# Kernel optimization log

Hardware: AMD Instinct MI355X
Metric: run time of the kernel (lower is better)

The kernel has to match this reference:

```python
import jax, jax.numpy as jnp
import numpy as np

R_S, R_C, P, L, NVOX, CH = 48, 144, 27, 2, 128, 128


def encode(x, L=L):
    # NeRF-style positional encoding: [sin(2^l x), cos(2^l x)] for l in range(L)
    feats = []
    for l in range(L):
        f = (2.0 ** l) * x
        feats.append(jnp.sin(f))
        feats.append(jnp.cos(f))
    return jnp.concatenate(feats, axis=-1)


def setup_inputs() -> dict:
    key = jax.random.key(0)
    ks = jax.random.split(key, 8)
    Np = 524288
    xyz = jax.random.uniform(ks[0], (Np, 3), dtype=jnp.float32)          # inside bbox [0,1]^3
    directions = jax.random.normal(ks[1], (Np, 3), dtype=jnp.float32)
    # voxel grid buffer: linspace over bbox per axis -> (3, NVOX)
    voxel = jnp.stack([jnp.linspace(0.0, 1.0, NVOX)] * 3, axis=0).astype(jnp.float32)
    sigma = 0.1 * jax.random.normal(ks[2], (3, R_S, NVOX), dtype=jnp.float32)
    feature = 0.1 * jax.random.normal(ks[3], (3, R_C, NVOX), dtype=jnp.float32)
    B = jax.random.normal(ks[4], (R_C, P), dtype=jnp.float32)
    din = (P + 3) * L * 2  # 120
    W1 = jax.random.normal(ks[5], (din, CH), dtype=jnp.float32) / jnp.sqrt(din)
    b1 = jnp.zeros((CH,), jnp.float32)
    W2 = jax.random.normal(ks[6], (CH, CH), dtype=jnp.float32) / jnp.sqrt(CH)
    b2 = jnp.zeros((CH,), jnp.float32)
    W3 = jax.random.normal(ks[7], (CH, 3), dtype=jnp.float32) / jnp.sqrt(CH)
    b3 = jnp.zeros((3,), jnp.float32)
    return {"xyz": xyz, "directions": directions, "voxel": voxel, "sigma": sigma,
            "feature": feature, "B": B, "W1": W1, "b1": b1, "W2": W2, "b2": b2,
            "W3": W3, "b3": b3}


def reference(xyz, directions, voxel, sigma, feature, B, W1, b1, W2, b2, W3, b3):
    SIGMA_BIAS = -5.0
    x = xyz.T  # (3, Np)
    Nv = voxel.shape[1]
    # snap_to_voxels: per-axis searchsorted + clamp + gather of grid coords
    inds = jax.vmap(jnp.searchsorted)(voxel, x)           # (3, Np)
    il = jnp.clip(inds - 1, 0, Nv - 1)
    ir = jnp.clip(inds, 0, Nv - 1)
    vl = jnp.take_along_axis(voxel, il, axis=1)           # (3, Np)
    vr = jnp.take_along_axis(voxel, ir, axis=1)
    w = (x - vl) / (vr - vl + 1e-6)                       # (3, Np) lerp weights

    # density: gather (3,R_s,Np), lerp, prod over axes(xyz), sum over rank
    sl = jnp.take_along_axis(sigma, il[:, None, :], axis=2)
    sr = jnp.take_along_axis(sigma, ir[:, None, :], axis=2)
    s = sl + (sr - sl) * w[:, None, :]                    # (3, R_s, Np)
    sigmas = jnp.sum(jnp.prod(s, axis=0), axis=0)         # (Np,)
    sigmas = jax.nn.softplus(sigmas + SIGMA_BIAS)

    # features: same pattern on (3,R_c,Np), then small matmul with B
    fl = jnp.take_along_axis(feature, il[:, None, :], axis=2)
    fr = jnp.take_along_axis(feature, ir[:, None, :], axis=2)
    f = fl + (fr - fl) * w[:, None, :]                    # (3, R_c, Np)
    feats = jnp.einsum('rn,rp->np', jnp.prod(f, axis=0), B)  # (Np, P)

    h = jnp.concatenate([encode(feats, L), encode(directions, L)], axis=1)  # (Np, 120)
    h = jax.nn.leaky_relu(h @ W1 + b1, negative_slope=0.01)
    h = jax.nn.leaky_relu(h @ W2 + b2, negative_slope=0.01)
    rgb = jax.nn.sigmoid(h @ W3 + b3)                     # (Np, 3)
    return sigmas, rgb
```

## Files before the change

### kernel.cpp

```cpp
#include <hip/hip_runtime.h>
#include <cstdint>

constexpr int RS  = 48;
constexpr int RC  = 144;
constexpr int PP  = 27;
constexpr int NV  = 128;
constexpr int CHN = 128;

constexpr int SIG_D  = 3 * NV * 64;
constexpr int FEAT_D = 3 * NV * 160;
constexpr int NPAIR  = SIG_D + FEAT_D;
constexpr int FR_B  = 0;
constexpr int FR_W1 = 5120;
constexpr int FR_W2 = 21504;
constexpr int FR_W3 = 37888;
constexpr int FR_TOT = 39936;

typedef __attribute__((ext_vector_type(8))) short short8;
typedef __attribute__((ext_vector_type(4))) float f32x4;
typedef __attribute__((ext_vector_type(2))) unsigned int u32x2;
typedef __attribute__((ext_vector_type(4))) unsigned int u32x4;
typedef _Float16 h2 __attribute__((ext_vector_type(2)));

__device__ __forceinline__ short f2bf(float f) {
    unsigned int u = __builtin_bit_cast(unsigned int, f);
    u += 0x7fffu + ((u >> 16) & 1u);
    return (short)(u >> 16);
}
__device__ __forceinline__ unsigned int pk2bf(float a, float b) {
    unsigned short ua = __builtin_bit_cast(unsigned short, (__bf16)a);
    unsigned short ub = __builtin_bit_cast(unsigned short, (__bf16)b);
    return (unsigned int)ua | ((unsigned int)ub << 16);
}
__device__ __forceinline__ float dot2lerp(unsigned int lodelta, h2 wv) {
#if __has_builtin(__builtin_amdgcn_fdot2)
    return __builtin_amdgcn_fdot2(__builtin_bit_cast(h2, lodelta), wv, 0.f, false);
#else
    h2 a = __builtin_bit_cast(h2, lodelta);
    return (float)a.x * (float)wv.x + (float)a.y * (float)wv.y;
#endif
}

__global__ void prep_tables(const float* __restrict__ sigma, const float* __restrict__ feature,
                            unsigned int* __restrict__ wt) {
    int idx = blockIdx.x * 256 + threadIdx.x;
    if (idx >= NPAIR) return;
    float lo = 0.f, hi = 0.f;
    if (idx < SIG_D) {
        int a = idx / 8192, t = idx % 8192;
        int v = t / 64, r = t % 64;
        if (r < RS) {
            lo = sigma[(a * RS + r) * NV + v];
            hi = sigma[(a * RS + r) * NV + min(v + 1, NV - 1)];
        }
    } else {
        int j = idx - SIG_D;
        int a = j / 20480, t = j % 20480;
        int v = t / 160, r = t % 160;
        if (r < RC) {
            lo = feature[(a * RC + r) * NV + v];
            hi = feature[(a * RC + r) * NV + min(v + 1, NV - 1)];
        }
    }
    _Float16 lh = (_Float16)lo;
    _Float16 dh = (_Float16)(hi - lo);
    wt[idx] = (unsigned int)__builtin_bit_cast(unsigned short, lh) |
              ((unsigned int)__builtin_bit_cast(unsigned short, dh) << 16);
}

__global__ void prep_frags(const float* __restrict__ Bm, const float* __restrict__ W1,
                           const float* __restrict__ W2, const float* __restrict__ W3,
                           short* __restrict__ fr) {
    int idx = blockIdx.x * 256 + threadIdx.x;
    if (idx >= FR_TOT) return;
    float val = 0.f;
    if (idx < FR_W1) {
        int j = idx - FR_B;
        int frag = j >> 9, li = (j >> 3) & 63, e = j & 7;
        int kt = frag >> 1, nt = frag & 1;
        int k = kt * 32 + (li >> 4) * 8 + e;
        int n = nt * 16 + (li & 15);
        val = (k < RC && n < PP) ? Bm[k * PP + n] : 0.f;
    } else if (idx < FR_W2) {
        int j = idx - FR_W1;
        int frag = j >> 9, li = (j >> 3) & 63, e = j & 7;
        int kt = frag >> 3, nt = frag & 7;
        int kn = kt * 32 + (li >> 4) * 8 + e;
        int n = nt * 16 + (li & 15);
        if (kn < 120) {
            int ko;
            if (kn < 108) { ko = (kn & 3) * PP + (kn >> 2); }
            else { int t2 = kn - 108; ko = 108 + (t2 & 3) * 3 + (t2 >> 2); }
            val = W1[ko * CHN + n];
        }
    } else if (idx < FR_W3) {
        int j = idx - FR_W2;
        int frag = j >> 9, li = (j >> 3) & 63, e = j & 7;
        int kt = frag >> 3, nt = frag & 7;
        int k = kt * 32 + (li >> 4) * 8 + e;
        int n = nt * 16 + (li & 15);
        val = W2[k * CHN + n];
    } else {
        int j = idx - FR_W3;
        int frag = j >> 9, li = (j >> 3) & 63, e = j & 7;
        int kt = frag;
        int k = kt * 32 + (li >> 4) * 8 + e;
        int n = li & 15;
        val = (n < 3) ? W3[k * 3 + n] : 0.f;
    }
    fr[idx] = f2bf(val);
}

__device__ __forceinline__ void lerpf8(const unsigned int* rl, h2 wv, float* pr, bool first) {
    u32x4 A  = *(const u32x4*)rl;
    u32x4 Bv = *(const u32x4*)(rl + 4);
#pragma unroll
    for (int d = 0; d < 4; ++d) {
        float s0 = dot2lerp(A[d], wv);
        float s1 = dot2lerp(Bv[d], wv);
        if (first) { pr[d] = s0; pr[4 + d] = s1; }
        else       { pr[d] *= s0; pr[4 + d] *= s1; }
    }
}

__global__ __launch_bounds__(128, 4)
void tensorf_main(const float* __restrict__ xyz, const float* __restrict__ dird,
                  const float* __restrict__ voxel,
                  const float* __restrict__ b1, const float* __restrict__ b2,
                  const float* __restrict__ b3,
                  const unsigned int* __restrict__ wt, const short* __restrict__ fr,
                  float* __restrict__ out, int Np) {
    __shared__ float voxs[3 * NV];
    __shared__ char  X[2 * 32 * 256];

    const int tid = threadIdx.x;
    const int wid = tid >> 6;
    const int lane = tid & 63;
    const int quad = lane >> 4, lane16 = lane & 15;
    const int wavebase = blockIdx.x * 64 + wid * 32;
    char* Xw = X + wid * 32 * 256;

    for (int i = tid; i < 3 * NV; i += 128) voxs[i] = voxel[i];
    __syncthreads();

    const unsigned int* SIGU  = wt;
    const unsigned int* FEATU = wt + SIG_D;
    const short* BFr = fr + FR_B;

#pragma unroll 1
    for (int q = 0; q < 2; ++q) {
        const int rowbase = q * 16;
        const int p = wavebase + rowbase + lane16;

        int ipb[3]; h2 wv[3];
#pragma unroll
        for (int a = 0; a < 3; ++a) {
            float x = xyz[p * 3 + a];
            int ind = (int)ceilf(x * 127.f);
            ind = min(max(ind, 0), 128);
            while (ind > 0 && voxs[a * NV + ind - 1] >= x) --ind;
            while (ind < 128 && voxs[a * NV + ind] < x) ++ind;
            int il = min(max(ind - 1, 0), 127);
            int ir = min(ind, 127);
            float vl = voxs[a * NV + il], vr = voxs[a * NV + ir];
            float w = (x - vl) / (vr - vl + 1e-6f);
            w = (il == 127) ? 1.f : w;
            ipb[a] = min(il, 126);
            wv[a] = h2{(_Float16)1.0f, (_Float16)w};
        }

        float sig = 0.f;
#pragma unroll
        for (int kt = 0; kt < 2; ++kt) {
            float pr[8];
#pragma unroll
            for (int a = 0; a < 3; ++a)
                lerpf8(SIGU + (a * NV + ipb[a]) * 64 + kt * 32 + quad * 8, wv[a], pr, a == 0);
#pragma unroll
            for (int j = 0; j < 8; ++j) sig += pr[j];
        }
        sig += __shfl_xor(sig, 16);
        sig += __shfl_xor(sig, 32);
        if (lane < 16) out[p] = log1pf(expf(sig - 5.f));

        f32x4 acc0 = {0.f, 0.f, 0.f, 0.f}, acc1 = {0.f, 0.f, 0.f, 0.f};
#pragma unroll
        for (int kt = 0; kt < 5; ++kt) {
            float pr[8];
#pragma unroll
            for (int a = 0; a < 3; ++a)
                lerpf8(FEATU + (a * NV + ipb[a]) * 160 + kt * 32 + quad * 8, wv[a], pr, a == 0);
            u32x4 uu;
#pragma unroll
            for (int d = 0; d < 4; ++d) uu[d] = pk2bf(pr[2 * d], pr[2 * d + 1]);
            short8 af = __builtin_bit_cast(short8, uu);
            short8 bf0 = *(const short8*)(BFr + ((kt * 2 + 0) * 64 + lane) * 8);
            short8 bf1 = *(const short8*)(BFr + ((kt * 2 + 1) * 64 + lane) * 8);
            acc0 = __builtin_amdgcn_mfma_f32_16x16x32_bf16(af, bf0, acc0, 0, 0, 0);
            acc1 = __builtin_amdgcn_mfma_f32_16x16x32_bf16(af, bf1, acc1, 0, 0, 0);
        }

#pragma unroll
        for (int nt = 0; nt < 2; ++nt) {
            int c = nt * 16 + lane16;
            f32x4 A = nt ? acc1 : acc0;
            if (c < PP) {
#pragma unroll
                for (int j = 0; j < 4; ++j) {
                    int row = rowbase + quad * 4 + j;
                    float f = A[j];
                    float s1 = __sinf(f), c1 = __cosf(f);
                    float s2 = 2.f * s1 * c1;
                    float c2 = fmaf(-2.f * s1, s1, 1.f);
                    unsigned int w0 = pk2bf(s1, c1);
                    unsigned int w1 = pk2bf(s2, c2);
                    int byte = c * 8;
                    int chunk = byte >> 4, off = byte & 15;
                    *(u32x2*)(Xw + row * 256 + ((chunk ^ (row & 7)) << 4) + off) = u32x2{w0, w1};
                }
            }
        }
        {
            int row = rowbase + lane16;
            if (quad < 3) {
                float d = dird[p * 3 + quad];
                float s1 = __sinf(d), c1 = __cosf(d);
                float s2 = 2.f * s1 * c1;
                float c2 = fmaf(-2.f * s1, s1, 1.f);
                unsigned int w0 = pk2bf(s1, c1);
                unsigned int w1 = pk2bf(s2, c2);
                int byte = 216 + 8 * quad;
                int chunk = byte >> 4, off = byte & 15;
                *(u32x2*)(Xw + row * 256 + ((chunk ^ (row & 7)) << 4) + off) = u32x2{w0, w1};
            } else {
                int addr = row * 256 + ((15 ^ (row & 7)) << 4);
                *(u32x4*)(Xw + addr) = u32x4{0u, 0u, 0u, 0u};
            }
        }
    }
    __syncthreads();

    const short* W1F = fr + FR_W1;
    const short* W2F = fr + FR_W2;
    const short* W3F = fr + FR_W3;

#pragma unroll 1
    for (int layer = 0; layer < 2; ++layer) {
        const short* WF = layer ? W2F : W1F;
        const float* bb = layer ? b2 : b1;

        short8 af[2][4];
#pragma unroll
        for (int m = 0; m < 2; ++m)
#pragma unroll
            for (int kt = 0; kt < 4; ++kt) {
                int row = m * 16 + lane16;
                int chunk = kt * 4 + quad;
                af[m][kt] = *(const short8*)(Xw + row * 256 + ((chunk ^ (row & 7)) << 4));
            }

#pragma unroll 1
        for (int nt = 0; nt < 8; ++nt) {
            short8 wfv[4];
#pragma unroll
            for (int kt = 0; kt < 4; ++kt)
                wfv[kt] = *(const short8*)(WF + ((kt * 8 + nt) * 64 + lane) * 8);
            f32x4 acc[2];
#pragma unroll
            for (int m = 0; m < 2; ++m) acc[m] = {0.f, 0.f, 0.f, 0.f};
#pragma unroll
            for (int m = 0; m < 2; ++m)
#pragma unroll
                for (int kt = 0; kt < 4; ++kt)
                    acc[m] = __builtin_amdgcn_mfma_f32_16x16x32_bf16(af[m][kt], wfv[kt], acc[m], 0, 0, 0);

            float bvv = bb[nt * 16 + lane16];
#pragma unroll
            for (int m = 0; m < 2; ++m) {
#pragma unroll
                for (int j = 0; j < 4; ++j) {
                    float v = acc[m][j] + bvv;
                    v = fmaxf(v, 0.01f * v);
                    int row = m * 16 + quad * 4 + j;
                    int byte = (nt * 16 + lane16) * 2;
                    int chunk = byte >> 4, off = byte & 15;
                    *(short*)(Xw + row * 256 + ((chunk ^ (row & 7)) << 4) + off) =
                        (short)__builtin_bit_cast(unsigned short, (__bf16)v);
                }
            }
        }
        __syncthreads();
    }

    {
        short8 af[2][4];
#pragma unroll
        for (int m = 0; m < 2; ++m)
#pragma unroll
            for (int kt = 0; kt < 4; ++kt) {
                int row = m * 16 + lane16;
                int chunk = kt * 4 + quad;
                af[m][kt] = *(const short8*)(Xw + row * 256 + ((chunk ^ (row & 7)) << 4));
            }
        short8 wf3[4];
#pragma unroll
        for (int kt = 0; kt < 4; ++kt)
            wf3[kt] = *(const short8*)(W3F + (kt * 64 + lane) * 8);

        f32x4 acc3[2];
#pragma unroll
        for (int m = 0; m < 2; ++m) acc3[m] = {0.f, 0.f, 0.f, 0.f};
#pragma unroll
        for (int m = 0; m < 2; ++m)
#pragma unroll
            for (int kt = 0; kt < 4; ++kt)
                acc3[m] = __builtin_amdgcn_mfma_f32_16x16x32_bf16(af[m][kt], wf3[kt], acc3[m], 0, 0, 0);

        if (lane16 < 3) {
            float bvv = b3[lane16];
#pragma unroll
            for (int m = 0; m < 2; ++m) {
#pragma unroll
                for (int j = 0; j < 4; ++j) {
                    float v = acc3[m][j] + bvv;
                    float r = 1.f / (1.f + expf(-v));
                    int row = m * 16 + quad * 4 + j;
                    out[Np + (wavebase + row) * 3 + lane16] = r;
                }
            }
        }
    }
}

extern "C" void kernel_launch(void* const* d_in, const int* in_sizes, int n_in,
                              void* d_out, int out_size, void* d_ws, size_t ws_size,
                              hipStream_t stream) {
    (void)n_in; (void)out_size; (void)ws_size;
    const float* xyz      = (const float*)d_in[0];
    const float* dird     = (const float*)d_in[1];
    const float* voxel    = (const float*)d_in[2];
    const float* sigma    = (const float*)d_in[3];
    const float* feature  = (const float*)d_in[4];
    const float* Bm       = (const float*)d_in[5];
    const float* W1       = (const float*)d_in[6];
    const float* b1       = (const float*)d_in[7];
    const float* W2       = (const float*)d_in[8];
    const float* b2       = (const float*)d_in[9];
    const float* W3       = (const float*)d_in[10];
    const float* b3       = (const float*)d_in[11];
    float* out = (float*)d_out;
    unsigned int* wt = (unsigned int*)d_ws;
    short* frg = (short*)d_ws + 2 * (size_t)NPAIR;

    const int Np = in_sizes[0] / 3;

    prep_tables<<<(NPAIR + 255) / 256, 256, 0, stream>>>(sigma, feature, wt);
    prep_frags<<<(FR_TOT + 255) / 256, 256, 0, stream>>>(Bm, W1, W2, W3, frg);
    tensorf_main<<<Np / 64, 128, 0, stream>>>(xyz, dird, voxel, b1, b2, b3, wt, frg, out, Np);
}
```

Before: 215.1 us.

## Split fused kernel into gather phase and MLP phase via workspace buffer

The fused kernel is split into two kernels. The first does the voxel lookup, density and feature projection, and writes 32 bf16 values per point (27 features plus 3 directions) to a workspace buffer. The second reads them back, computes the sin/cos encoding in registers, and runs the three MLP layers with one 16-row tile per wave. Each kernel should get lighter register and LDS use and so higher occupancy. In exchange it adds a global round trip of about 64 bytes per point and an extra launch. It also stores the raw features in bf16 before encoding, which may cost precision in the sin/cos inputs. The fused path is kept as a fallback when the workspace is too small.

```diff
diff --git a/kernel.cpp b/kernel.cpp
--- a/kernel.cpp
+++ b/kernel.cpp
@@ -32,6 +32,8 @@
     unsigned short ub = __builtin_bit_cast(unsigned short, (__bf16)b);
     return (unsigned int)ua | ((unsigned int)ub << 16);
 }
+__device__ __forceinline__ float bflo(unsigned int u) { return __builtin_bit_cast(float, u << 16); }
+__device__ __forceinline__ float bfhi(unsigned int u) { return __builtin_bit_cast(float, u & 0xffff0000u); }
 __device__ __forceinline__ float dot2lerp(unsigned int lodelta, h2 wv) {
 #if __has_builtin(__builtin_amdgcn_fdot2)
     return __builtin_amdgcn_fdot2(__builtin_bit_cast(h2, lodelta), wv, 0.f, false);
@@ -123,13 +125,190 @@
     }
 }
 
+__global__ __launch_bounds__(256, 6)
+void phaseA(const float* __restrict__ xyz, const float* __restrict__ dird,
+            const float* __restrict__ voxel,
+            const unsigned int* __restrict__ wt, const short* __restrict__ fr,
+            float* __restrict__ out, unsigned short* __restrict__ X64, int Np) {
+    __shared__ float voxs[3 * NV];
+    const int tid = threadIdx.x;
+    const int wid = tid >> 6;
+    const int lane = tid & 63;
+    const int quad = lane >> 4, lane16 = lane & 15;
+    const int wavebase = blockIdx.x * 64 + wid * 16;
+    const int p = wavebase + lane16;
+
+    for (int i = tid; i < 3 * NV; i += 256) voxs[i] = voxel[i];
+    __syncthreads();
+
+    const unsigned int* SIGU  = wt;
+    const unsigned int* FEATU = wt + SIG_D;
+    const short* BFr = fr + FR_B;
+
+    int ipb[3]; h2 wv[3];
+#pragma unroll
+    for (int a = 0; a < 3; ++a) {
+        float x = xyz[p * 3 + a];
+        int ind = (int)ceilf(x * 127.f);
+        ind = min(max(ind, 0), 128);
+        while (ind > 0 && voxs[a * NV + ind - 1] >= x) --ind;
+        while (ind < 128 && voxs[a * NV + ind] < x) ++ind;
+        int il = min(max(ind - 1, 0), 127);
+        int ir = min(ind, 127);
+        float vl = voxs[a * NV + il], vr = voxs[a * NV + ir];
+        float w = (x - vl) / (vr - vl + 1e-6f);
+        w = (il == 127) ? 1.f : w;
+        ipb[a] = min(il, 126);
+        wv[a] = h2{(_Float16)1.0f, (_Float16)w};
+    }
+
+    float sig = 0.f;
+#pragma unroll
+    for (int kt = 0; kt < 2; ++kt) {
+        float pr[8];
+#pragma unroll
+        for (int a = 0; a < 3; ++a)
+            lerpf8(SIGU + (a * NV + ipb[a]) * 64 + kt * 32 + quad * 8, wv[a], pr, a == 0);
+#pragma unroll
+        for (int j = 0; j < 8; ++j) sig += pr[j];
+    }
+    sig += __shfl_xor(sig, 16);
+    sig += __shfl_xor(sig, 32);
+    if (lane < 16) out[p] = log1pf(expf(sig - 5.f));
+
+    f32x4 acc0 = {0.f, 0.f, 0.f, 0.f}, acc1 = {0.f, 0.f, 0.f, 0.f};
+#pragma unroll
+    for (int kt = 0; kt < 5; ++kt) {
+        float pr[8];
+#pragma unroll
+        for (int a = 0; a < 3; ++a)
+            lerpf8(FEATU + (a * NV + ipb[a]) * 160 + kt * 32 + quad * 8, wv[a], pr, a == 0);
+        u32x4 uu;
+#pragma unroll
+        for (int d = 0; d < 4; ++d) uu[d] = pk2bf(pr[2 * d], pr[2 * d + 1]);
+        short8 af = __builtin_bit_cast(short8, uu);
+        short8 bf0 = *(const short8*)(BFr + ((kt * 2 + 0) * 64 + lane) * 8);
+        short8 bf1 = *(const short8*)(BFr + ((kt * 2 + 1) * 64 + lane) * 8);
+        acc0 = __builtin_amdgcn_mfma_f32_16x16x32_bf16(af, bf0, acc0, 0, 0, 0);
+        acc1 = __builtin_amdgcn_mfma_f32_16x16x32_bf16(af, bf1, acc1, 0, 0, 0);
+    }
+
+#pragma unroll
+    for (int nt = 0; nt < 2; ++nt) {
+        int c = nt * 16 + lane16;
+        f32x4 A = nt ? acc1 : acc0;
+        if (c < PP) {
+#pragma unroll
+            for (int j = 0; j < 4; ++j) {
+                int prow = wavebase + quad * 4 + j;
+                X64[prow * 32 + c] = (unsigned short)__builtin_bit_cast(unsigned short, (__bf16)A[j]);
+            }
+        }
+    }
+    if (quad < 3) {
+        float d = dird[p * 3 + quad];
+        X64[p * 32 + 27 + quad] = (unsigned short)__builtin_bit_cast(unsigned short, (__bf16)d);
+    } else {
+        *(unsigned int*)(X64 + p * 32 + 30) = 0u;
+    }
+}
+
+__global__ __launch_bounds__(256, 8)
+void phaseB(const unsigned short* __restrict__ X64, const short* __restrict__ fr,
+            const float* __restrict__ b1, const float* __restrict__ b2,
+            const float* __restrict__ b3, float* __restrict__ out, int Np) {
+    __shared__ char T[4 * 16 * 256];
+    const int tid = threadIdx.x;
+    const int wid = tid >> 6;
+    const int lane = tid & 63;
+    const int quad = lane >> 4, lane16 = lane & 15;
+    const int rowbase = blockIdx.x * 64 + wid * 16;
+    char* Tw = T + wid * 16 * 256;
+
+    const short* W1F = fr + FR_W1;
+    const short* W2F = fr + FR_W2;
+    const short* W3F = fr + FR_W3;
+
+    short8 af[4];
+#pragma unroll
+    for (int kt = 0; kt < 4; ++kt) {
+        unsigned int d = *(const unsigned int*)(X64 + (rowbase + lane16) * 32 + kt * 8 + quad * 2);
+        float f0 = bflo(d), f1 = bfhi(d);
+        float s1 = __sinf(f0), c1 = __cosf(f0);
+        float s2 = 2.f * s1 * c1, c2 = fmaf(-2.f * s1, s1, 1.f);
+        float s1b = __sinf(f1), c1b = __cosf(f1);
+        float s2b = 2.f * s1b * c1b, c2b = fmaf(-2.f * s1b, s1b, 1.f);
+        u32x4 uu = {pk2bf(s1, c1), pk2bf(s2, c2), pk2bf(s1b, c1b), pk2bf(s2b, c2b)};
+        af[kt] = __builtin_bit_cast(short8, uu);
+    }
+
+#pragma unroll 1
+    for (int layer = 0; layer < 2; ++layer) {
+        const short* WF = layer ? W2F : W1F;
+        const float* bb = layer ? b2 : b1;
+#pragma unroll 1
+        for (int nt = 0; nt < 8; ++nt) {
+            short8 wfv[4];
+#pragma unroll
+            for (int kt = 0; kt < 4; ++kt)
+                wfv[kt] = *(const short8*)(WF + ((kt * 8 + nt) * 64 + lane) * 8);
+            f32x4 acc = {0.f, 0.f, 0.f, 0.f};
+#pragma unroll
+            for (int kt = 0; kt < 4; ++kt)
+                acc = __builtin_amdgcn_mfma_f32_16x16x32_bf16(af[kt], wfv[kt], acc, 0, 0, 0);
+
+            float bvv = bb[nt * 16 + lane16];
+#pragma unroll
+            for (int j = 0; j < 4; ++j) {
+                float v = acc[j] + bvv;
+                v = fmaxf(v, 0.01f * v);
+                int row = quad * 4 + j;
+                int byte = (nt * 16 + lane16) * 2;
+                int chunk = byte >> 4, off = byte & 15;
+                *(short*)(Tw + row * 256 + ((chunk ^ (row & 7)) << 4) + off) =
+                    (short)__builtin_bit_cast(unsigned short, (__bf16)v);
+            }
+        }
+        __syncthreads();
+#pragma unroll
+        for (int kt = 0; kt < 4; ++kt) {
+            int row = lane16;
+            int chunk = kt * 4 + quad;
+            af[kt] = *(const short8*)(Tw + row * 256 + ((chunk ^ (row & 7)) << 4));
+        }
+        __syncthreads();
+    }
+
+    {
+        short8 wf3[4];
+#pragma unroll
+        for (int kt = 0; kt < 4; ++kt)
+            wf3[kt] = *(const short8*)(W3F + (kt * 64 + lane) * 8);
+        f32x4 acc3 = {0.f, 0.f, 0.f, 0.f};
+#pragma unroll
+        for (int kt = 0; kt < 4; ++kt)
+            acc3 = __builtin_amdgcn_mfma_f32_16x16x32_bf16(af[kt], wf3[kt], acc3, 0, 0, 0);
+
+        if (lane16 < 3) {
+            float bvv = b3[lane16];
+#pragma unroll
+            for (int j = 0; j < 4; ++j) {
+                float v = acc3[j] + bvv;
+                float r = 1.f / (1.f + expf(-v));
+                int row = quad * 4 + j;
+                out[Np + (rowbase + row) * 3 + lane16] = r;
+            }
+        }
+    }
+}
+
 __global__ __launch_bounds__(128, 4)
-void tensorf_main(const float* __restrict__ xyz, const float* __restrict__ dird,
-                  const float* __restrict__ voxel,
-                  const float* __restrict__ b1, const float* __restrict__ b2,
-                  const float* __restrict__ b3,
-                  const unsigned int* __restrict__ wt, const short* __restrict__ fr,
-                  float* __restrict__ out, int Np) {
+void tensorf_fused(const float* __restrict__ xyz, const float* __restrict__ dird,
+                   const float* __restrict__ voxel,
+                   const float* __restrict__ b1, const float* __restrict__ b2,
+                   const float* __restrict__ b3,
+                   const unsigned int* __restrict__ wt, const short* __restrict__ fr,
+                   float* __restrict__ out, int Np) {
     __shared__ float voxs[3 * NV];
     __shared__ char  X[2 * 32 * 256];
 
@@ -151,7 +330,6 @@
     for (int q = 0; q < 2; ++q) {
         const int rowbase = q * 16;
         const int p = wavebase + rowbase + lane16;
-
         int ipb[3]; h2 wv[3];
 #pragma unroll
         for (int a = 0; a < 3; ++a) {
@@ -168,7 +346,6 @@
             ipb[a] = min(il, 126);
             wv[a] = h2{(_Float16)1.0f, (_Float16)w};
         }
-
         float sig = 0.f;
 #pragma unroll
         for (int kt = 0; kt < 2; ++kt) {
@@ -199,7 +376,6 @@
             acc0 = __builtin_amdgcn_mfma_f32_16x16x32_bf16(af, bf0, acc0, 0, 0, 0);
             acc1 = __builtin_amdgcn_mfma_f32_16x16x32_bf16(af, bf1, acc1, 0, 0, 0);
         }
-
 #pragma unroll
         for (int nt = 0; nt < 2; ++nt) {
             int c = nt * 16 + lane16;
@@ -248,7 +424,6 @@
     for (int layer = 0; layer < 2; ++layer) {
         const short* WF = layer ? W2F : W1F;
         const float* bb = layer ? b2 : b1;
-
         short8 af[2][4];
 #pragma unroll
         for (int m = 0; m < 2; ++m)
@@ -258,7 +433,6 @@
                 int chunk = kt * 4 + quad;
                 af[m][kt] = *(const short8*)(Xw + row * 256 + ((chunk ^ (row & 7)) << 4));
             }
-
 #pragma unroll 1
         for (int nt = 0; nt < 8; ++nt) {
             short8 wfv[4];
@@ -273,7 +447,6 @@
 #pragma unroll
                 for (int kt = 0; kt < 4; ++kt)
                     acc[m] = __builtin_amdgcn_mfma_f32_16x16x32_bf16(af[m][kt], wfv[kt], acc[m], 0, 0, 0);
-
             float bvv = bb[nt * 16 + lane16];
 #pragma unroll
             for (int m = 0; m < 2; ++m) {
@@ -291,7 +464,6 @@
         }
         __syncthreads();
     }
-
     {
         short8 af[2][4];
 #pragma unroll
@@ -306,7 +478,6 @@
 #pragma unroll
         for (int kt = 0; kt < 4; ++kt)
             wf3[kt] = *(const short8*)(W3F + (kt * 64 + lane) * 8);
-
         f32x4 acc3[2];
 #pragma unroll
         for (int m = 0; m < 2; ++m) acc3[m] = {0.f, 0.f, 0.f, 0.f};
@@ -315,7 +486,6 @@
 #pragma unroll
             for (int kt = 0; kt < 4; ++kt)
                 acc3[m] = __builtin_amdgcn_mfma_f32_16x16x32_bf16(af[m][kt], wf3[kt], acc3[m], 0, 0, 0);
-
         if (lane16 < 3) {
             float bvv = b3[lane16];
 #pragma unroll
@@ -335,7 +505,7 @@
 extern "C" void kernel_launch(void* const* d_in, const int* in_sizes, int n_in,
                               void* d_out, int out_size, void* d_ws, size_t ws_size,
                               hipStream_t stream) {
-    (void)n_in; (void)out_size; (void)ws_size;
+    (void)n_in; (void)out_size;
     const float* xyz      = (const float*)d_in[0];
     const float* dird     = (const float*)d_in[1];
     const float* voxel    = (const float*)d_in[2];
@@ -353,8 +523,17 @@
     short* frg = (short*)d_ws + 2 * (size_t)NPAIR;
 
     const int Np = in_sizes[0] / 3;
+    const size_t base = (size_t)NPAIR * 4 + (size_t)FR_TOT * 2;
+    const size_t need = base + (size_t)Np * 64;
 
     prep_tables<<<(NPAIR + 255) / 256, 256, 0, stream>>>(sigma, feature, wt);
     prep_frags<<<(FR_TOT + 255) / 256, 256, 0, stream>>>(Bm, W1, W2, W3, frg);
-    tensorf_main<<<Np / 64, 128, 0, stream>>>(xyz, dird, voxel, b1, b2, b3, wt, frg, out, Np);
-}
+
+    if (ws_size >= need) {
+        unsigned short* X64 = (unsigned short*)((char*)d_ws + base);
+        phaseA<<<Np / 64, 256, 0, stream>>>(xyz, dird, voxel, wt, frg, out, X64, Np);
+        phaseB<<<Np / 64, 256, 0, stream>>>(X64, frg, b1, b2, b3, out, Np);
+    } else {
+        tensorf_fused<<<Np / 64, 128, 0, stream>>>(xyz, dird, voxel, b1, b2, b3, wt, frg, out, Np);
+    }
+}
```

Measured after the change: 260.7 us. +21.2%, slower.
